# Kernel optimization log

Hardware: AMD Instinct MI355X
Metric: run time of the kernel (lower is better)

The kernel has to match this reference:

```python
import jax, jax.numpy as jnp
import numpy as np

HIDDEN = 2048
H = 16            # num heads
Q_RANK = 1536
KV_RANK = 512
D_NOPE = 128
D_ROPE = 64
D_QK = D_NOPE + D_ROPE   # 192
D_V = 128
ROPE_BASE = 10000.0
EPS = 1e-6


def _rms_norm(x, w):
    xf = x.astype(jnp.float32)
    var = jnp.mean(xf * xf, axis=-1, keepdims=True)
    return w * (xf * jax.lax.rsqrt(var + EPS)).astype(x.dtype)


def _rotate_half(x):
    x1, x2 = x[..., : x.shape[-1] // 2], x[..., x.shape[-1] // 2:]
    return jnp.concatenate((-x2, x1), axis=-1)


def _rope_cos_sin(position_ids, dtype):
    inv_freq = 1.0 / (ROPE_BASE ** (jnp.arange(0, D_ROPE, 2, dtype=jnp.float32) / D_ROPE))
    freqs = position_ids.astype(jnp.float32)[..., None] * inv_freq  # [b,s,32]
    emb = jnp.concatenate((freqs, freqs), axis=-1)                  # [b,s,64]
    return jnp.cos(emb).astype(dtype), jnp.sin(emb).astype(dtype)


def setup_inputs() -> dict:
    key = jax.random.key(0)
    ks = jax.random.split(key, 8)
    b, s = 1, 2048
    scale = 0.02
    return {
        "hidden_states": jax.random.normal(ks[0], (b, s, HIDDEN), jnp.float32),
        "position_ids": jnp.broadcast_to(jnp.arange(s, dtype=jnp.int64)[None, :], (b, s)),
        "q_a_w": jax.random.normal(ks[1], (Q_RANK, HIDDEN), jnp.float32) * scale,
        "q_a_ln_w": jnp.ones((Q_RANK,), jnp.float32),
        "q_b_w": jax.random.normal(ks[2], (H * D_QK, Q_RANK), jnp.float32) * scale,
        "kv_a_w": jax.random.normal(ks[3], (KV_RANK + D_ROPE, HIDDEN), jnp.float32) * scale,
        "kv_a_ln_w": jnp.ones((KV_RANK,), jnp.float32),
        "kv_b_w": jax.random.normal(ks[4], (H * (D_NOPE + D_V), KV_RANK), jnp.float32) * scale,
        "o_w": jax.random.normal(ks[5], (HIDDEN, H * D_V), jnp.float32) * scale,
    }


def reference(hidden_states, position_ids, q_a_w, q_a_ln_w, q_b_w, kv_a_w, kv_a_ln_w, kv_b_w, o_w):
    b, s, _ = hidden_states.shape
    softmax_scale = D_QK ** (-0.5)

    # Q path: low-rank down-proj -> RMSNorm -> up-proj
    q_a = hidden_states @ q_a_w.T                              # [b,s,q_rank]
    q = (_rms_norm(q_a, q_a_ln_w) @ q_b_w.T).reshape(b, s, H, D_QK)
    q_nope, q_pe = q[..., :D_NOPE], q[..., D_NOPE:]

    # KV path: joint down-proj -> split latent / rope part
    kv_a = hidden_states @ kv_a_w.T                            # [b,s,kv_rank+rope]
    compressed_kv = _rms_norm(kv_a[..., :KV_RANK], kv_a_ln_w)  # [b,s,kv_rank]
    k_pe = kv_a[..., KV_RANK:]                                 # [b,s,rope]
    kv_b = (compressed_kv @ kv_b_w.T).reshape(b, s, H, D_NOPE + D_V)
    k_nope, v = kv_b[..., :D_NOPE], kv_b[..., D_NOPE:]

    # decoupled RoPE on the rope slice
    cos, sin = _rope_cos_sin(position_ids, hidden_states.dtype)  # [b,s,64]
    cos, sin = cos[:, :, None, :], sin[:, :, None, :]            # [b,s,1,64]
    q_pe = q_pe * cos + _rotate_half(q_pe) * sin                 # [b,s,H,64]
    k_pe_h = jnp.broadcast_to(k_pe[:, :, None, :], (b, s, H, D_ROPE))
    k_pe_h = k_pe_h * cos + _rotate_half(k_pe_h) * sin

    q_full = jnp.concatenate([q_nope, q_pe], axis=-1)            # [b,s,H,192]
    k_full = jnp.concatenate([k_nope, k_pe_h], axis=-1)          # [b,s,H,192]

    # naive materialized attention (matches reference)
    scores = jnp.einsum("bqhd,bkhd->bhqk", q_full, k_full) * softmax_scale
    causal = jnp.triu(jnp.full((s, s), -jnp.inf, dtype=scores.dtype), k=1)
    scores = scores + causal
    probs = jax.nn.softmax(scores.astype(jnp.float32), axis=-1).astype(q_full.dtype)
    attn = jnp.einsum("bhqk,bkhd->bqhd", probs, v).reshape(b, s, H * D_V)
    return attn @ o_w.T
```

## Files before the change

### kernel.cpp

```cpp
#include <hip/hip_runtime.h>
#include <stdint.h>

#define S_LEN 2048
#define HIDDEN_ 2048
#define NH 16
#define QR 1536
#define KVR 512
#define DN 128
#define DR 64
#define DQK 192
#define DV 128

typedef __attribute__((ext_vector_type(8))) short bf16x8;
typedef __attribute__((ext_vector_type(4))) float f32x4;
typedef __attribute__((ext_vector_type(4))) unsigned short u16x4;
typedef unsigned short u16;
typedef unsigned int u32;

#define GLOAD_LDS16(g, l)                                                      \
    __builtin_amdgcn_global_load_lds(                                          \
        (const __attribute__((address_space(1))) void*)(g),                    \
        (__attribute__((address_space(3))) void*)(l), 16, 0, 0)

__device__ inline float bf2f(u16 x) {
    union { u32 u; float f; } v; v.u = ((u32)x) << 16; return v.f;
}
__device__ inline u16 f2bf(float f) {
    union { float f; u32 u; } v; v.f = f;
    u32 u = v.u;
    return (u16)((u + 0x7fffu + ((u >> 16) & 1u)) >> 16);
}

__global__ void cvt_multi(const float* s0, u16* d0, int n0,
                          const float* s1, u16* d1, int n1,
                          const float* s2, u16* d2, int n2,
                          const float* s3, u16* d3, int n3,
                          const float* s4, u16* d4, int n4,
                          const float* s5, u16* d5, int n5)
{
    const float* src; u16* dst; int n;
    switch (blockIdx.y) {
        case 0: src = s0; dst = d0; n = n0; break;
        case 1: src = s1; dst = d1; n = n1; break;
        case 2: src = s2; dst = d2; n = n2; break;
        case 3: src = s3; dst = d3; n = n3; break;
        case 4: src = s4; dst = d4; n = n4; break;
        default: src = s5; dst = d5; n = n5; break;
    }
    int i = (blockIdx.x * 256 + threadIdx.x) * 4;
    if (i + 3 < n) {
        float4 v = *(const float4*)(src + i);
        dst[i + 0] = f2bf(v.x);
        dst[i + 1] = f2bf(v.y);
        dst[i + 2] = f2bf(v.z);
        dst[i + 3] = f2bf(v.w);
    }
}

__device__ __forceinline__
void gemm_body(const u16* __restrict__ A, const u16* __restrict__ B,
               void* __restrict__ Cv, int M, int N, int K, int out_f32,
               int bx, int by)
{
    __shared__ u16 sA[128 * 32];
    __shared__ u16 sB[128 * 32];
    const int tid  = threadIdx.x;
    const int wave = tid >> 6;
    const int lane = tid & 63;
    const int l16  = lane & 15;
    const int quad = lane >> 4;
    const int m_blk = by * 128;
    const int n_blk = bx * 128;
    const int wm = (wave >> 1) * 64;
    const int wn = (wave & 1) * 64;

    const f32x4 zero4 = {0.f, 0.f, 0.f, 0.f};
    f32x4 acc[4][4];
#pragma unroll
    for (int i = 0; i < 4; i++)
#pragma unroll
        for (int j = 0; j < 4; j++) acc[i][j] = zero4;

    const int srow = lane >> 2;
    const int scol = (lane & 3) * 8;

    for (int k0 = 0; k0 < K; k0 += 32) {
        __syncthreads();
#pragma unroll
        for (int p = 0; p < 2; p++) {
            const int rbase = wave * 32 + p * 16;
            const int row = rbase + srow;
            const u16* ga = A + (size_t)(m_blk + row) * K + k0 + scol;
            GLOAD_LDS16(ga, &sA[rbase * 32]);
            int brow = n_blk + row; if (brow >= N) brow = N - 1;
            const u16* gb = B + (size_t)brow * K + k0 + scol;
            GLOAD_LDS16(gb, &sB[rbase * 32]);
        }
        __syncthreads();

        bf16x8 af[4], bfr[4];
#pragma unroll
        for (int i = 0; i < 4; i++)
            af[i] = *(const bf16x8*)(sA + (wm + i * 16 + l16) * 32 + quad * 8);
#pragma unroll
        for (int j = 0; j < 4; j++)
            bfr[j] = *(const bf16x8*)(sB + (wn + j * 16 + l16) * 32 + quad * 8);
#pragma unroll
        for (int i = 0; i < 4; i++)
#pragma unroll
            for (int j = 0; j < 4; j++)
                acc[i][j] = __builtin_amdgcn_mfma_f32_16x16x32_bf16(
                    af[i], bfr[j], acc[i][j], 0, 0, 0);
    }

#pragma unroll
    for (int i = 0; i < 4; i++)
#pragma unroll
        for (int j = 0; j < 4; j++)
#pragma unroll
            for (int r = 0; r < 4; r++) {
                int mrow = m_blk + wm + i * 16 + quad * 4 + r;
                int ncol = n_blk + wn + j * 16 + l16;
                if (ncol < N) {
                    if (out_f32)
                        ((float*)Cv)[(size_t)mrow * N + ncol] = acc[i][j][r];
                    else
                        ((u16*)Cv)[(size_t)mrow * N + ncol] = f2bf(acc[i][j][r]);
                }
            }
}

__global__ __launch_bounds__(256, 3)
void gemm_bt(const u16* __restrict__ A, const u16* __restrict__ B,
             void* __restrict__ Cv, int M, int N, int K, int out_f32)
{
    gemm_body(A, B, Cv, M, N, K, out_f32, blockIdx.x, blockIdx.y);
}

__global__ __launch_bounds__(256, 3)
void gemm_dual(const u16* A0, const u16* B0, u16* C0, int M0, int N0, int K0,
               const u16* A1, const u16* B1, u16* C1, int M1, int N1, int K1)
{
    if (blockIdx.z == 0) {
        if ((int)blockIdx.x >= (N0 + 127) / 128) return;
        gemm_body(A0, B0, C0, M0, N0, K0, 0, blockIdx.x, blockIdx.y);
    } else {
        gemm_body(A1, B1, C1, M1, N1, K1, 0, blockIdx.x, blockIdx.y);
    }
}

__global__ void rmsnorm2_k(const u16* __restrict__ X0, const float* __restrict__ W0,
                           u16* __restrict__ Y0,
                           const u16* __restrict__ X1, const float* __restrict__ W1,
                           u16* __restrict__ Y1, int in_stride)
{
    const u16* X; const float* W; u16* Y; int len, out_stride;
    if (blockIdx.y == 0) { X = X0; W = W0; Y = Y0; len = QR;  out_stride = QR; }
    else                 { X = X1; W = W1; Y = Y1; len = KVR; out_stride = KVR; }
    const int row = blockIdx.x;
    const u16* x = X + (size_t)row * in_stride;
    u16* y = Y + (size_t)row * out_stride;
    float ss = 0.f;
    for (int i = threadIdx.x; i < len; i += 256) { float v = bf2f(x[i]); ss += v * v; }
#pragma unroll
    for (int off = 32; off; off >>= 1) ss += __shfl_down(ss, off, 64);
    __shared__ float red[4];
    if ((threadIdx.x & 63) == 0) red[threadIdx.x >> 6] = ss;
    __syncthreads();
    float tot = red[0] + red[1] + red[2] + red[3];
    float inv = 1.0f / sqrtf(tot / (float)len + 1e-6f);
    for (int i = threadIdx.x; i < len; i += 256)
        y[i] = f2bf(W[i] * bf2f(x[i]) * inv);
}

__global__ void rope_repack(const u16* __restrict__ q,
                            const u16* __restrict__ kvb,
                            const u16* __restrict__ kva_pe,
                            int kva_stride,
                            u16* __restrict__ Q, u16* __restrict__ Kf)
{
    const int s = blockIdx.x;
    const float pos = (float)s;
    const int t = threadIdx.x;
    __shared__ float cs[64], sn[64];
    __shared__ u16 kpe_r[64];
    if (t < 64) {
        int jf = t & 31;
        float freq = powf(10000.f, -(float)(2 * jf) / 64.f);
        float ang = pos * freq;
        cs[t] = cosf(ang);
        sn[t] = sinf(ang);
    }
    __syncthreads();
    if (t < 64) {
        int j = t;
        float x = bf2f(kva_pe[(size_t)s * kva_stride + j]);
        float other = (j < 32) ? -bf2f(kva_pe[(size_t)s * kva_stride + j + 32])
                               :  bf2f(kva_pe[(size_t)s * kva_stride + j - 32]);
        kpe_r[j] = f2bf(x * cs[j] + other * sn[j]);
    }
    __syncthreads();

    for (int idx = t; idx < NH * DQK; idx += 256) {
        int h = idx / DQK, d = idx % DQK;
        const size_t qrow = (size_t)s * (NH * DQK) + h * DQK;
        u16 qv;
        if (d < DN) qv = q[qrow + d];
        else {
            int j = d - DN;
            float x = bf2f(q[qrow + DN + j]);
            float other = (j < 32) ? -bf2f(q[qrow + DN + j + 32])
                                   :  bf2f(q[qrow + DN + j - 32]);
            qv = f2bf(x * cs[j] + other * sn[j]);
        }
        Q[((size_t)h * S_LEN + s) * DQK + d] = qv;
        u16 kv;
        if (d < DN) kv = kvb[(size_t)s * (NH * 256) + h * 256 + d];
        else        kv = kpe_r[d - DN];
        Kf[((size_t)h * S_LEN + s) * DQK + d] = kv;
    }
}

__global__ void transpose_v(const u16* __restrict__ kvb, u16* __restrict__ Vt)
{
    __shared__ u16 tile[64][72];
    const int h  = blockIdx.z;
    const int s0 = blockIdx.x * 64;
    const int d0 = blockIdx.y * 64;
    const int t  = threadIdx.x;
#pragma unroll
    for (int p = 0; p < 2; p++) {
        int c = p * 256 + t;
        int r = c >> 3, col = (c & 7) * 8;
        *(bf16x8*)&tile[r][col] =
            *(const bf16x8*)&kvb[(size_t)(s0 + r) * (NH * 256) + h * 256 + 128 + d0 + col];
    }
    __syncthreads();
#pragma unroll
    for (int p = 0; p < 2; p++) {
        int c = p * 256 + t;
        int dr = c >> 3, sc = (c & 7) * 8;
        bf16x8 v;
#pragma unroll
        for (int j = 0; j < 8; j++) v[j] = (short)tile[sc + j][dr];
        *(bf16x8*)&Vt[((size_t)h * DV + d0 + dr) * S_LEN + s0 + sc] = v;
    }
}

__global__ __launch_bounds__(256, 2)
void mla_attn(const u16* __restrict__ Q, const u16* __restrict__ Kf,
              const u16* __restrict__ Vt, u16* __restrict__ attn,
              float* __restrict__ part)
{
    const int h  = blockIdx.y;
    const int bx = blockIdx.x;
    int s, tb, te, cIdx; bool direct;
    if (bx < 16)      { s = 16 + bx; tb = 0;  te = 32;        cIdx = 0; direct = false; }
    else if (bx < 32) { s = 47 - bx; tb = 32; te = 2 * s + 2; cIdx = 1; direct = false; }
    else              { s = 47 - bx; tb = 0;  te = 2 * s + 2; cIdx = 0; direct = true;  }

    const int wave  = threadIdx.x >> 6;
    const int lane  = threadIdx.x & 63;
    const int l16   = lane & 15;
    const int quad  = lane >> 4;
    const int q0    = s * 64 + wave * 16;
    const int qrow  = q0 + l16;

    const u16* Qh  = Q  + (size_t)h * S_LEN * DQK;
    const u16* Kh  = Kf + (size_t)h * S_LEN * DQK;
    const u16* Vth = Vt + (size_t)h * DV * S_LEN;

    __shared__ u16 sK[2][24 * 32 * 8];
    __shared__ u16 sV[2][4 * 128 * 8];
    __shared__ u16 pbuf[4][16][36];
    u16 (*pb)[36] = pbuf[wave];

    bf16x8 qf[6];
#pragma unroll
    for (int st = 0; st < 6; st++)
        qf[st] = *(const bf16x8*)(Qh + (size_t)qrow * DQK + st * 32 + quad * 8);

    const f32x4 zero4 = {0.f, 0.f, 0.f, 0.f};
    f32x4 oacc[8];
#pragma unroll
    for (int t = 0; t < 8; t++) oacc[t] = zero4;
    float mrow = -INFINITY, lrow = 0.f;

    const float scale = 0.07216878364870323f;

    auto stage = [&](int buf, int c0) {
#pragma unroll
        for (int g = 0; g < 3; g++) {
            int c = g * 256 + wave * 64 + lane;
            int row = c & 31, cg = c >> 5;
            GLOAD_LDS16(Kh + (size_t)(c0 + row) * DQK + cg * 8,
                        &sK[buf][(g * 256 + wave * 64) * 8]);
        }
#pragma unroll
        for (int g = 0; g < 2; g++) {
            int c = g * 256 + wave * 64 + lane;
            int d = c & 127, cg = c >> 7;
            GLOAD_LDS16(Vth + (size_t)d * S_LEN + c0 + cg * 8,
                        &sV[buf][(g * 256 + wave * 64) * 8]);
        }
    };

    stage(0, tb * 32);

    for (int kt = tb; kt < te; kt++) {
        const int c0  = kt * 32;
        const int cur = (kt - tb) & 1;
        __syncthreads();
        if (kt + 1 < te) stage(cur ^ 1, c0 + 32);

        if (c0 <= q0 + 15) {
            f32x4 s0 = zero4, s1 = zero4;
#pragma unroll
            for (int st = 0; st < 6; st++) {
                bf16x8 k0 = *(const bf16x8*)&sK[cur][((st * 4 + quad) * 32 + l16) * 8];
                bf16x8 k1 = *(const bf16x8*)&sK[cur][((st * 4 + quad) * 32 + 16 + l16) * 8];
                s0 = __builtin_amdgcn_mfma_f32_16x16x32_bf16(k0, qf[st], s0, 0, 0, 0);
                s1 = __builtin_amdgcn_mfma_f32_16x16x32_bf16(k1, qf[st], s1, 0, 0, 0);
            }
            bf16x8 vfr[8];
#pragma unroll
            for (int t = 0; t < 8; t++)
                vfr[t] = *(const bf16x8*)&sV[cur][(quad * 128 + t * 16 + l16) * 8];

            const bool full = (c0 + 31 <= q0);
            float v0[4], v1[4];
#pragma unroll
            for (int r = 0; r < 4; r++) {
                v0[r] = s0[r] * scale;
                v1[r] = s1[r] * scale;
                if (!full) {
                    if (c0 + quad * 4 + r > qrow)      v0[r] = -INFINITY;
                    if (c0 + 16 + quad * 4 + r > qrow) v1[r] = -INFINITY;
                }
            }
            float lm = fmaxf(fmaxf(fmaxf(v0[0], v0[1]), fmaxf(v0[2], v0[3])),
                             fmaxf(fmaxf(v1[0], v1[1]), fmaxf(v1[2], v1[3])));
            lm = fmaxf(lm, __shfl_xor(lm, 16, 64));
            lm = fmaxf(lm, __shfl_xor(lm, 32, 64));
            const float mnew  = fmaxf(mrow, lm);
            const float alpha = __expf(mrow - mnew);
            float p0[4], p1[4], rs = 0.f;
#pragma unroll
            for (int r = 0; r < 4; r++) {
                p0[r] = __expf(v0[r] - mnew);
                p1[r] = __expf(v1[r] - mnew);
                rs += p0[r] + p1[r];
            }
            rs += __shfl_xor(rs, 16, 64);
            rs += __shfl_xor(rs, 32, 64);
            lrow = lrow * alpha + rs;
            mrow = mnew;
#pragma unroll
            for (int t = 0; t < 8; t++) oacc[t] *= alpha;

            u16x4 pk0, pk1;
#pragma unroll
            for (int r = 0; r < 4; r++) { pk0[r] = f2bf(p0[r]); pk1[r] = f2bf(p1[r]); }
            *(u16x4*)&pb[l16][quad * 4]      = pk0;
            *(u16x4*)&pb[l16][16 + quad * 4] = pk1;
            asm volatile("s_waitcnt lgkmcnt(0)" ::: "memory");
            bf16x8 pfrag = *(const bf16x8*)(&pb[l16][quad * 8]);

#pragma unroll
            for (int t = 0; t < 8; t++)
                oacc[t] = __builtin_amdgcn_mfma_f32_16x16x32_bf16(vfr[t], pfrag,
                                                                  oacc[t], 0, 0, 0);
        }
    }

    if (direct) {
        const float linv = 1.0f / lrow;
#pragma unroll
        for (int t = 0; t < 8; t++) {
            u16x4 ov;
#pragma unroll
            for (int r = 0; r < 4; r++) ov[r] = f2bf(oacc[t][r] * linv);
            *(u16x4*)&attn[(size_t)qrow * (NH * DV) + h * DV + t * 16 + quad * 4] = ov;
        }
    } else {
        float* pout = part + ((size_t)(h * 16 + (s - 16)) * 2 + cIdx) * 8320;
        const int rowl = wave * 16 + l16;
#pragma unroll
        for (int t = 0; t < 8; t++) {
            float4 ov = {oacc[t][0], oacc[t][1], oacc[t][2], oacc[t][3]};
            *(float4*)&pout[(size_t)rowl * 128 + t * 16 + quad * 4] = ov;
        }
        if (quad == 0) {
            pout[8192 + rowl] = mrow;
            pout[8256 + rowl] = lrow;
        }
    }
}

__global__ void attn_combine(const float* __restrict__ part, u16* __restrict__ attn)
{
    const int h = blockIdx.y, sIdx = blockIdx.x;
    const int s = 16 + sIdx;
    const float* p0 = part + ((size_t)(h * 16 + sIdx) * 2 + 0) * 8320;
    const float* p1 = p0 + 8320;
    for (int e = threadIdx.x; e < 8192; e += 256) {
        int row = e >> 7, d = e & 127;
        float m0 = p0[8192 + row], m1 = p1[8192 + row];
        float l0 = p0[8256 + row], l1 = p1[8256 + row];
        float M  = fmaxf(m0, m1);
        float w0 = __expf(m0 - M), w1 = __expf(m1 - M);
        float o  = (w0 * p0[e] + w1 * p1[e]) / (w0 * l0 + w1 * l1);
        attn[(size_t)(s * 64 + row) * (NH * DV) + h * DV + d] = f2bf(o);
    }
}

extern "C" void kernel_launch(void* const* d_in, const int* in_sizes, int n_in,
                              void* d_out, int out_size, void* d_ws, size_t ws_size,
                              hipStream_t stream)
{
    const float* hid      = (const float*)d_in[0];
    const float* q_a_w    = (const float*)d_in[2];
    const float* q_a_ln_w = (const float*)d_in[3];
    const float* q_b_w    = (const float*)d_in[4];
    const float* kv_a_w   = (const float*)d_in[5];
    const float* kv_a_ln_w= (const float*)d_in[6];
    const float* kv_b_w   = (const float*)d_in[7];
    const float* o_w      = (const float*)d_in[8];

    const int NQKV = QR + KVR + DR;

    char* base = (char*)d_ws;
    u16* qkvaw_b = (u16*)(base + 0);
    u16* qbw_b   = (u16*)(base + 8650752);
    u16* kvbw_b  = (u16*)(base + 18087936);
    u16* ow_b    = (u16*)(base + 22282240);
    u16* hid_b   = (u16*)(base + 30670848);
    u16* qkv_a   = (u16*)(base + 39059456);
    u16* q_n     = (u16*)(base + 47710208);
    u16* ckv     = (u16*)(base + 54001664);
    u16* qb      = (u16*)(base + 56098816);
    u16* kvb     = (u16*)(base + 68681728);
    u16* Qb      = (u16*)(base + 85458944);
    u16* Kb      = (u16*)(base + 98041856);
    u16* Vtb     = (u16*)(base + 110624768);
    u16* attnb   = (u16*)(base + 39059456);
    float* partb = (float*)(base + 56098816);

    cvt_multi<<<dim3(4608, 6), 256, 0, stream>>>(
        hid,    hid_b,                          HIDDEN_ * S_LEN,
        q_a_w,  qkvaw_b,                        QR * HIDDEN_,
        kv_a_w, qkvaw_b + (size_t)QR * HIDDEN_, (KVR + DR) * HIDDEN_,
        q_b_w,  qbw_b,                          NH * DQK * QR,
        kv_b_w, kvbw_b,                         NH * 256 * KVR,
        o_w,    ow_b,                           HIDDEN_ * NH * DV);

    gemm_bt<<<dim3((NQKV + 127) / 128, S_LEN / 128), 256, 0, stream>>>(
        hid_b, qkvaw_b, qkv_a, S_LEN, NQKV, HIDDEN_, 0);
    rmsnorm2_k<<<dim3(S_LEN, 2), 256, 0, stream>>>(
        qkv_a, q_a_ln_w, q_n, qkv_a + QR, kv_a_ln_w, ckv, NQKV);
    gemm_dual<<<dim3(32, S_LEN / 128, 2), 256, 0, stream>>>(
        q_n, qbw_b, qb,  S_LEN, NH * DQK, QR,
        ckv, kvbw_b, kvb, S_LEN, NH * 256, KVR);
    rope_repack<<<S_LEN, 256, 0, stream>>>(qb, kvb, qkv_a + QR + KVR, NQKV, Qb, Kb);
    transpose_v<<<dim3(S_LEN / 64, DV / 64, NH), 256, 0, stream>>>(kvb, Vtb);
    mla_attn<<<dim3(48, NH), 256, 0, stream>>>(Qb, Kb, Vtb, attnb, partb);
    attn_combine<<<dim3(16, NH), 256, 0, stream>>>(partb, attnb);
    gemm_bt<<<dim3(HIDDEN_ / 128, S_LEN / 128), 256, 0, stream>>>(
        attnb, ow_b, (float*)d_out, S_LEN, HIDDEN_, HIDDEN_, 1);
}
```

Baseline: 366.9 us.

## Split-K the down-projection and output GEMMs, fusing partial sums into RMSNorm

The QKV down-projection and output projection GEMMs now split K in two along a grid z dimension. Each half writes an fp32 partial buffer. For the down-projection the two partials are summed inside the RMSNorm kernel, which also emits the rope slice as bf16. For the output projection a separate vector add kernel sums them. This doubles the block count on GEMMs that otherwise launch only about 256-272 blocks, at the cost of extra fp32 traffic and one more kernel. The change also vectorises the bf16 stores in the conversion kernel, raises the attention kernel's launch_bounds occupancy hint from 2 to 3, and reorganises the workspace layout.

```diff
diff --git a/kernel.cpp b/kernel.cpp
--- a/kernel.cpp
+++ b/kernel.cpp
@@ -10,6 +10,7 @@
 #define DR 64
 #define DQK 192
 #define DV 128
+#define NQKV 2112
 
 typedef __attribute__((ext_vector_type(8))) short bf16x8;
 typedef __attribute__((ext_vector_type(4))) float f32x4;
@@ -50,17 +51,16 @@
     int i = (blockIdx.x * 256 + threadIdx.x) * 4;
     if (i + 3 < n) {
         float4 v = *(const float4*)(src + i);
-        dst[i + 0] = f2bf(v.x);
-        dst[i + 1] = f2bf(v.y);
-        dst[i + 2] = f2bf(v.z);
-        dst[i + 3] = f2bf(v.w);
+        u16x4 o;
+        o[0] = f2bf(v.x); o[1] = f2bf(v.y); o[2] = f2bf(v.z); o[3] = f2bf(v.w);
+        *(u16x4*)(dst + i) = o;
     }
 }
 
 __device__ __forceinline__
 void gemm_body(const u16* __restrict__ A, const u16* __restrict__ B,
-               void* __restrict__ Cv, int M, int N, int K, int out_f32,
-               int bx, int by)
+               void* __restrict__ Cv, int M, int N, int Kloop, int ld,
+               int out_f32, int bx, int by)
 {
     __shared__ u16 sA[128 * 32];
     __shared__ u16 sB[128 * 32];
@@ -84,16 +84,16 @@
     const int srow = lane >> 2;
     const int scol = (lane & 3) * 8;
 
-    for (int k0 = 0; k0 < K; k0 += 32) {
+    for (int k0 = 0; k0 < Kloop; k0 += 32) {
         __syncthreads();
 #pragma unroll
         for (int p = 0; p < 2; p++) {
             const int rbase = wave * 32 + p * 16;
             const int row = rbase + srow;
-            const u16* ga = A + (size_t)(m_blk + row) * K + k0 + scol;
+            const u16* ga = A + (size_t)(m_blk + row) * ld + k0 + scol;
             GLOAD_LDS16(ga, &sA[rbase * 32]);
             int brow = n_blk + row; if (brow >= N) brow = N - 1;
-            const u16* gb = B + (size_t)brow * K + k0 + scol;
+            const u16* gb = B + (size_t)brow * ld + k0 + scol;
             GLOAD_LDS16(gb, &sB[rbase * 32]);
         }
         __syncthreads();
@@ -131,10 +131,13 @@
 }
 
 __global__ __launch_bounds__(256, 3)
-void gemm_bt(const u16* __restrict__ A, const u16* __restrict__ B,
-             void* __restrict__ Cv, int M, int N, int K, int out_f32)
-{
-    gemm_body(A, B, Cv, M, N, K, out_f32, blockIdx.x, blockIdx.y);
+void gemm_splitk(const u16* __restrict__ A, const u16* __restrict__ B,
+                 float* __restrict__ C0, float* __restrict__ C1,
+                 int M, int N, int Kh, int ld)
+{
+    float* C = blockIdx.z ? C1 : C0;
+    gemm_body(A + (size_t)blockIdx.z * Kh, B + (size_t)blockIdx.z * Kh,
+              C, M, N, Kh, ld, 1, blockIdx.x, blockIdx.y);
 }
 
 __global__ __launch_bounds__(256, 3)
@@ -143,40 +146,48 @@
 {
     if (blockIdx.z == 0) {
         if ((int)blockIdx.x >= (N0 + 127) / 128) return;
-        gemm_body(A0, B0, C0, M0, N0, K0, 0, blockIdx.x, blockIdx.y);
+        gemm_body(A0, B0, C0, M0, N0, K0, K0, 0, blockIdx.x, blockIdx.y);
     } else {
-        gemm_body(A1, B1, C1, M1, N1, K1, 0, blockIdx.x, blockIdx.y);
-    }
-}
-
-__global__ void rmsnorm2_k(const u16* __restrict__ X0, const float* __restrict__ W0,
-                           u16* __restrict__ Y0,
-                           const u16* __restrict__ X1, const float* __restrict__ W1,
-                           u16* __restrict__ Y1, int in_stride)
-{
-    const u16* X; const float* W; u16* Y; int len, out_stride;
-    if (blockIdx.y == 0) { X = X0; W = W0; Y = Y0; len = QR;  out_stride = QR; }
-    else                 { X = X1; W = W1; Y = Y1; len = KVR; out_stride = KVR; }
+        gemm_body(A1, B1, C1, M1, N1, K1, K1, 0, blockIdx.x, blockIdx.y);
+    }
+}
+
+__global__ void rmsnorm2_k(const float* __restrict__ P0, const float* __restrict__ P1,
+                           const float* __restrict__ W0, u16* __restrict__ Y0,
+                           const float* __restrict__ W1, u16* __restrict__ Y1,
+                           u16* __restrict__ kpe)
+{
     const int row = blockIdx.x;
-    const u16* x = X + (size_t)row * in_stride;
-    u16* y = Y + (size_t)row * out_stride;
+    const float* p0 = P0 + (size_t)row * NQKV;
+    const float* p1 = P1 + (size_t)row * NQKV;
+    __shared__ float xbuf[QR];
+    __shared__ float red[4];
+    int off, len; const float* W; u16* Y;
+    if (blockIdx.y == 0) { off = 0;  len = QR;  W = W0; Y = Y0 + (size_t)row * QR;  }
+    else                 { off = QR; len = KVR; W = W1; Y = Y1 + (size_t)row * KVR; }
     float ss = 0.f;
-    for (int i = threadIdx.x; i < len; i += 256) { float v = bf2f(x[i]); ss += v * v; }
-#pragma unroll
-    for (int off = 32; off; off >>= 1) ss += __shfl_down(ss, off, 64);
-    __shared__ float red[4];
+    for (int i = threadIdx.x; i < len; i += 256) {
+        float v = p0[off + i] + p1[off + i];
+        xbuf[i] = v;
+        ss += v * v;
+    }
+#pragma unroll
+    for (int o = 32; o; o >>= 1) ss += __shfl_down(ss, o, 64);
     if ((threadIdx.x & 63) == 0) red[threadIdx.x >> 6] = ss;
     __syncthreads();
     float tot = red[0] + red[1] + red[2] + red[3];
     float inv = 1.0f / sqrtf(tot / (float)len + 1e-6f);
     for (int i = threadIdx.x; i < len; i += 256)
-        y[i] = f2bf(W[i] * bf2f(x[i]) * inv);
+        Y[i] = f2bf(W[i] * xbuf[i] * inv);
+    if (blockIdx.y == 1 && threadIdx.x < DR) {
+        int i = threadIdx.x;
+        kpe[(size_t)row * DR + i] = f2bf(p0[QR + KVR + i] + p1[QR + KVR + i]);
+    }
 }
 
 __global__ void rope_repack(const u16* __restrict__ q,
                             const u16* __restrict__ kvb,
-                            const u16* __restrict__ kva_pe,
-                            int kva_stride,
+                            const u16* __restrict__ kpe_b,
                             u16* __restrict__ Q, u16* __restrict__ Kf)
 {
     const int s = blockIdx.x;
@@ -194,9 +205,9 @@
     __syncthreads();
     if (t < 64) {
         int j = t;
-        float x = bf2f(kva_pe[(size_t)s * kva_stride + j]);
-        float other = (j < 32) ? -bf2f(kva_pe[(size_t)s * kva_stride + j + 32])
-                               :  bf2f(kva_pe[(size_t)s * kva_stride + j - 32]);
+        float x = bf2f(kpe_b[(size_t)s * DR + j]);
+        float other = (j < 32) ? -bf2f(kpe_b[(size_t)s * DR + j + 32])
+                               :  bf2f(kpe_b[(size_t)s * DR + j - 32]);
         kpe_r[j] = f2bf(x * cs[j] + other * sn[j]);
     }
     __syncthreads();
@@ -247,7 +258,7 @@
     }
 }
 
-__global__ __launch_bounds__(256, 2)
+__global__ __launch_bounds__(256, 3)
 void mla_attn(const u16* __restrict__ Q, const u16* __restrict__ Kf,
               const u16* __restrict__ Vt, u16* __restrict__ attn,
               float* __restrict__ part)
@@ -414,6 +425,18 @@
     }
 }
 
+__global__ void addf2(const float* __restrict__ a, const float* __restrict__ b,
+                      float* __restrict__ o, int n)
+{
+    int i = (blockIdx.x * 256 + threadIdx.x) * 4;
+    if (i + 3 < n) {
+        float4 va = *(const float4*)(a + i);
+        float4 vb = *(const float4*)(b + i);
+        float4 vo = {va.x + vb.x, va.y + vb.y, va.z + vb.z, va.w + vb.w};
+        *(float4*)(o + i) = vo;
+    }
+}
+
 extern "C" void kernel_launch(void* const* d_in, const int* in_sizes, int n_in,
                               void* d_out, int out_size, void* d_ws, size_t ws_size,
                               hipStream_t stream)
@@ -427,24 +450,26 @@
     const float* kv_b_w   = (const float*)d_in[7];
     const float* o_w      = (const float*)d_in[8];
 
-    const int NQKV = QR + KVR + DR;
-
     char* base = (char*)d_ws;
     u16* qkvaw_b = (u16*)(base + 0);
     u16* qbw_b   = (u16*)(base + 8650752);
     u16* kvbw_b  = (u16*)(base + 18087936);
     u16* ow_b    = (u16*)(base + 22282240);
     u16* hid_b   = (u16*)(base + 30670848);
-    u16* qkv_a   = (u16*)(base + 39059456);
-    u16* q_n     = (u16*)(base + 47710208);
-    u16* ckv     = (u16*)(base + 54001664);
-    u16* qb      = (u16*)(base + 56098816);
-    u16* kvb     = (u16*)(base + 68681728);
-    u16* Qb      = (u16*)(base + 85458944);
-    u16* Kb      = (u16*)(base + 98041856);
-    u16* Vtb     = (u16*)(base + 110624768);
-    u16* attnb   = (u16*)(base + 39059456);
-    float* partb = (float*)(base + 56098816);
+    float* P0    = (float*)(base + 39059456);
+    float* P1    = (float*)(base + 56360960);
+    u16* q_n     = (u16*)(base + 73662464);
+    u16* ckv     = (u16*)(base + 79953920);
+    u16* kpe_b   = (u16*)(base + 82051072);
+    u16* qb      = (u16*)(base + 82313216);
+    u16* kvb     = (u16*)(base + 94896128);
+    u16* Qb      = (u16*)(base + 39059456);
+    u16* Kb      = (u16*)(base + 51642368);
+    u16* Vtb     = (u16*)(base + 64225280);
+    u16* attnb   = (u16*)(base + 72613888);
+    float* partb = (float*)(base + 94896128);
+    float* PO0   = (float*)(base + 82313216);
+    float* PO1   = (float*)(base + 99090432);
 
     cvt_multi<<<dim3(4608, 6), 256, 0, stream>>>(
         hid,    hid_b,                          HIDDEN_ * S_LEN,
@@ -454,17 +479,19 @@
         kv_b_w, kvbw_b,                         NH * 256 * KVR,
         o_w,    ow_b,                           HIDDEN_ * NH * DV);
 
-    gemm_bt<<<dim3((NQKV + 127) / 128, S_LEN / 128), 256, 0, stream>>>(
-        hid_b, qkvaw_b, qkv_a, S_LEN, NQKV, HIDDEN_, 0);
+    gemm_splitk<<<dim3((NQKV + 127) / 128, S_LEN / 128, 2), 256, 0, stream>>>(
+        hid_b, qkvaw_b, P0, P1, S_LEN, NQKV, HIDDEN_ / 2, HIDDEN_);
     rmsnorm2_k<<<dim3(S_LEN, 2), 256, 0, stream>>>(
-        qkv_a, q_a_ln_w, q_n, qkv_a + QR, kv_a_ln_w, ckv, NQKV);
+        P0, P1, q_a_ln_w, q_n, kv_a_ln_w, ckv, kpe_b);
     gemm_dual<<<dim3(32, S_LEN / 128, 2), 256, 0, stream>>>(
         q_n, qbw_b, qb,  S_LEN, NH * DQK, QR,
         ckv, kvbw_b, kvb, S_LEN, NH * 256, KVR);
-    rope_repack<<<S_LEN, 256, 0, stream>>>(qb, kvb, qkv_a + QR + KVR, NQKV, Qb, Kb);
+    rope_repack<<<S_LEN, 256, 0, stream>>>(qb, kvb, kpe_b, Qb, Kb);
     transpose_v<<<dim3(S_LEN / 64, DV / 64, NH), 256, 0, stream>>>(kvb, Vtb);
     mla_attn<<<dim3(48, NH), 256, 0, stream>>>(Qb, Kb, Vtb, attnb, partb);
     attn_combine<<<dim3(16, NH), 256, 0, stream>>>(partb, attnb);
-    gemm_bt<<<dim3(HIDDEN_ / 128, S_LEN / 128), 256, 0, stream>>>(
-        attnb, ow_b, (float*)d_out, S_LEN, HIDDEN_, HIDDEN_, 1);
-}
+    gemm_splitk<<<dim3(HIDDEN_ / 128, S_LEN / 128, 2), 256, 0, stream>>>(
+        attnb, ow_b, PO0, PO1, S_LEN, HIDDEN_, HIDDEN_ / 2, HIDDEN_);
+    addf2<<<dim3((S_LEN * HIDDEN_) / 1024), 256, 0, stream>>>(
+        PO0, PO1, (float*)d_out, S_LEN * HIDDEN_);
+}
```

Measured after the change: 351.7 us. -4.1%, faster.
